# Optimization experiments

Hardware: AMD Instinct MI355X
Metric: run time of the kernel (lower is better)

The kernel has to match this reference:

```python
import jax, jax.numpy as jnp
import numpy as np

N, IN_DIM, HID_DIM, N_CLASSES, MLP_W = 4096, 256, 128, 2, 16


def setup_inputs() -> dict:
    key = jax.random.key(0)
    ks = jax.random.split(key, 8)
    u = jax.random.uniform(ks[0], (N, N), dtype=jnp.float32)
    adj = jnp.where(u < 0.01, 1.0, 0.0).astype(jnp.float32)
    deg_row = adj.sum(axis=1)  # [N]
    deg_col = adj.sum(axis=0)  # [N]
    # per-edge row/col degree features, materialized NxN as in the source
    xdeg = (jnp.broadcast_to(deg_row[:, None], (N, N)) * jnp.ones((1,), jnp.float32)).astype(jnp.float32)
    ydeg = (jnp.broadcast_to(deg_col[None, :], (N, N)) * jnp.ones((1,), jnp.float32)).astype(jnp.float32)
    x = jax.random.normal(ks[1], (N, IN_DIM), dtype=jnp.float32)
    s = 0.1
    We1 = jax.random.normal(ks[2], (3, MLP_W), dtype=jnp.float32) * s
    be1 = jnp.zeros((MLP_W,), jnp.float32)
    We2 = jax.random.normal(ks[3], (MLP_W, 2), dtype=jnp.float32) * s
    be2 = jnp.zeros((2,), jnp.float32)
    W1 = jax.random.normal(ks[4], (IN_DIM, HID_DIM), dtype=jnp.float32) * s
    b1 = jnp.zeros((HID_DIM,), jnp.float32)
    W2 = jax.random.normal(ks[5], (HID_DIM, N_CLASSES), dtype=jnp.float32) * s
    b2 = jnp.zeros((N_CLASSES,), jnp.float32)
    resid_weight = jnp.array(0.5, dtype=jnp.float32)  # learned scalar (init 0.0 in source)
    return {"x": x, "adj": adj, "xdeg": xdeg, "ydeg": ydeg,
            "We1": We1, "be1": be1, "We2": We2, "be2": be2,
            "W1": W1, "b1": b1, "W2": W2, "b2": b2,
            "resid_weight": resid_weight}


def reference(x, adj, xdeg, ydeg, We1, be1, We2, be2, W1, b1, W2, b2, resid_weight):
    n = adj.shape[0]
    # Edge-gating MLP over (adj, xdeg, ydeg). The source gathers nonzero entries,
    # runs the MLP, and scatters back into a zero tensor; computing densely and
    # masking by (adj != 0) is mathematically identical (adj * gate kills zeros).
    feats = jnp.stack([adj, xdeg, ydeg], axis=-1)            # [N, N, 3]
    h = jax.nn.relu(jnp.einsum('nmf,fw->nmw', feats, We1) + be1)  # [N, N, 16]
    gate = jax.nn.softmax(jnp.einsum('nmw,wc->nmc', h, We2) + be2, axis=-1)[..., 1]
    gate = jnp.where(adj != 0.0, gate, 0.0)
    A = adj * gate + jnp.eye(n, dtype=adj.dtype)             # reweighted + self-loops
    # Degree normalization: source does A @ D_col, transpose, @ D_row, transpose,
    # which equals drow[:,None] * A * dcol[None,:]; use broadcasting (no O(N^3) diag mm).
    rs = A.sum(axis=1)
    cs = A.sum(axis=0)
    drow = jnp.where(rs > 0, rs ** -0.5, 0.0)
    dcol = jnp.where(cs > 0, cs ** -0.5, 0.0)
    An = drow[:, None] * A * dcol[None, :]
    # Layer 1: propagate, residual, linear (nn1 = MLP([in, hid]) -> single Linear).
    out = An @ x + resid_weight * x
    hid = out @ W1 + b1
    # dropout is identity in eval mode
    # Layer 2: propagate, residual, classifier.
    out2 = An @ hid + resid_weight * hid
    return out2 @ W2 + b2
```

## Files before the change

kernel.cpp:

```cpp
#include <hip/hip_runtime.h>


typedef unsigned char u8;
typedef unsigned int  u32;

#define N_NODES 4096
#define MAX_DEG 128
#define LUTD    128

__global__ __launch_bounds__(256)
void k_prep(const float* __restrict__ We1, const float* __restrict__ be1,
            const float* __restrict__ We2, const float* __restrict__ be2,
            const float* __restrict__ W1,  const float* __restrict__ b1,
            const float* __restrict__ W2,  const float* __restrict__ b2,
            const float* __restrict__ xdeg, const float* __restrict__ ydeg,
            float* __restrict__ lut, float* __restrict__ M,
            float* __restrict__ cz, float* __restrict__ cfin,
            u8* __restrict__ dc_u8, u8* __restrict__ dr_u8,
            float* __restrict__ cs) {
    int b = blockIdx.x, tid = threadIdx.x;
    if (b < 64) {
        int e = b * 256 + tid;
        float dr = (float)(e >> 7), dc = (float)(e & 127);
        float delta = be2[1] - be2[0];
        #pragma unroll
        for (int w = 0; w < 16; ++w) {
            float hh = fmaf(We1[32 + w], dc,
                       fmaf(We1[16 + w], dr, We1[w] + be1[w]));
            hh = fmaxf(hh, 0.f);
            delta = fmaf(hh, We2[w * 2 + 1] - We2[w * 2], delta);
        }
        lut[e] = 1.f / (1.f + __expf(-delta));
    } else if (b < 66) {
        int e = (b - 64) * 256 + tid;
        int t = e >> 1, d = e & 1;
        float s = 0.f;
        for (int h = 0; h < 128; ++h)
            s = fmaf(W1[t * 128 + h], W2[h * 2 + d], s);
        M[e] = s;
    } else if (b == 66) {
        if (tid < 2) {
            float s = 0.f;
            for (int h = 0; h < 128; ++h)
                s = fmaf(b1[h], W2[h * 2 + tid], s);
            cz[tid]   = s;
            cfin[tid] = b2[tid];
        }
    } else if (b < 83) {
        int j = (b - 67) * 256 + tid;
        int d = (int)ydeg[j];
        dc_u8[j] = (u8)(d > 127 ? 127 : d);
        cs[j] = 0.f;
    } else {
        int i = (b - 83) * 256 + tid;
        int d = (int)xdeg[(size_t)i * N_NODES];
        dr_u8[i] = (u8)(d > 127 ? 127 : d);
    }
}

__global__ __launch_bounds__(256)
void k_gatey(const float* __restrict__ adj, const u8* __restrict__ dr_u8,
             const float* __restrict__ x, const float* __restrict__ lut,
             const u8* __restrict__ dc_u8, const float* __restrict__ M,
             int2* __restrict__ e_g, float* __restrict__ rs,
             float* __restrict__ cs, int* __restrict__ cnt,
             float* __restrict__ y) {
    __shared__ int   s_cnt;
    __shared__ float s_rs[4];
    const int i = blockIdx.x, tid = threadIdx.x;
    const int wv = tid >> 6, lane = tid & 63;
    if (tid == 0) s_cnt = 0;

    const float4* arow4 = (const float4*)(adj + (size_t)i * N_NODES);
    float4 v0 = arow4[tid * 4 + 0];
    float4 v1 = arow4[tid * 4 + 1];
    float4 v2 = arow4[tid * 4 + 2];
    float4 v3 = arow4[tid * 4 + 3];
    uint4  dcw = ((const uint4*)dc_u8)[tid];
    const float* lut_row = lut + (int)dr_u8[i] * LUTD;

    float p0 = 0.f, p1 = 0.f;
    if (wv == 0) {
        float4 xv  = ((const float4*)(x + (size_t)i * 256))[lane];
        float4 m01 = ((const float4*)M)[lane * 2 + 0];
        float4 m23 = ((const float4*)M)[lane * 2 + 1];
        p0 = xv.x * m01.x + xv.y * m01.z + xv.z * m23.x + xv.w * m23.z;
        p1 = xv.x * m01.y + xv.y * m01.w + xv.z * m23.y + xv.w * m23.w;
    }

    float vals[16] = {v0.x, v0.y, v0.z, v0.w, v1.x, v1.y, v1.z, v1.w,
                      v2.x, v2.y, v2.z, v2.w, v3.x, v3.y, v3.z, v3.w};
    u32 mask = 0;
    #pragma unroll
    for (int q = 0; q < 16; ++q)
        mask |= (vals[q] != 0.f) ? (1u << q) : 0u;

    float lrs = 0.f;
    int nloc = __popc(mask);
    if (nloc) {
        int pos = atomicAdd(&s_cnt, nloc);
        int2* er = e_g + (size_t)i * MAX_DEG;
        const u32 w[4] = {dcw.x, dcw.y, dcw.z, dcw.w};
        u32 m = mask;
        while (m) {
            int q = __ffs(m) - 1;
            m &= m - 1;
            int j = tid * 16 + q;
            float gate = lut_row[(w[q >> 2] >> ((q & 3) * 8)) & 255u];
            lrs += gate;
            atomicAdd(cs + j, gate);
            if (pos < MAX_DEG) er[pos] = make_int2(j, __float_as_int(gate));
            ++pos;
        }
    }

    #pragma unroll
    for (int o = 32; o > 0; o >>= 1) {
        lrs += __shfl_down(lrs, o);
        p0  += __shfl_down(p0, o);
        p1  += __shfl_down(p1, o);
    }
    if (lane == 0) s_rs[wv] = lrs;
    if (tid == 0)  ((float2*)y)[i] = make_float2(p0, p1);
    __syncthreads();
    if (tid == 0) {
        rs[i]  = 1.f + s_rs[0] + s_rs[1] + s_rs[2] + s_rs[3];
        cnt[i] = (s_cnt < MAX_DEG) ? s_cnt : MAX_DEG;
    }
}

__global__ __launch_bounds__(256)
void k_spmv(const int2* __restrict__ e_g, const int* __restrict__ cnt,
            const float* __restrict__ rs, const float* __restrict__ cs,
            const float* __restrict__ vin, const float* __restrict__ addv,
            const float* __restrict__ rw, float* __restrict__ vout) {
    int sub = threadIdx.x >> 5, lane32 = threadIdx.x & 31;
    int i = blockIdx.x * 8 + sub;
    int nnz = cnt[i];
    const int2* ep = e_g + (size_t)i * MAX_DEG;
    float a0 = 0.f, a1 = 0.f;
    for (int k = lane32; k < nnz; k += 32) {
        int2 e = ep[k];
        float2 vj = ((const float2*)vin)[e.x];
        float wt = __int_as_float(e.y) * rsqrtf(cs[e.x] + 1.f);
        a0 = fmaf(wt, vj.x, a0);
        a1 = fmaf(wt, vj.y, a1);
    }
    #pragma unroll
    for (int o = 16; o > 0; o >>= 1) {
        a0 += __shfl_down(a0, o, 32);
        a1 += __shfl_down(a1, o, 32);
    }
    if (lane32 == 0) {
        float r  = rw[0];
        float di = rsqrtf(rs[i]), ci = rsqrtf(cs[i] + 1.f);
        float2 yv = ((const float2*)vin)[i];
        float2 o;
        o.x = di * (a0 + ci * yv.x) + r * yv.x + addv[0];
        o.y = di * (a1 + ci * yv.y) + r * yv.y + addv[1];
        ((float2*)vout)[i] = o;
    }
}

extern "C" void kernel_launch(void* const* d_in, const int* in_sizes, int n_in,
                              void* d_out, int out_size, void* d_ws, size_t ws_size,
                              hipStream_t stream) {
    const float* x    = (const float*)d_in[0];
    const float* adj  = (const float*)d_in[1];
    const float* xdeg = (const float*)d_in[2];
    const float* ydeg = (const float*)d_in[3];
    const float* We1  = (const float*)d_in[4];
    const float* be1  = (const float*)d_in[5];
    const float* We2  = (const float*)d_in[6];
    const float* be2  = (const float*)d_in[7];
    const float* W1   = (const float*)d_in[8];
    const float* b1   = (const float*)d_in[9];
    const float* W2   = (const float*)d_in[10];
    const float* b2   = (const float*)d_in[11];
    const float* rw   = (const float*)d_in[12];

    char* ws = (char*)d_ws;
    int2*  e_g  = (int2*) (ws + 0);
    float* lut  = (float*)(ws + 4194304);
    float* rs   = (float*)(ws + 4259840);
    float* cs   = (float*)(ws + 4276224);
    int*   cnt  = (int*)  (ws + 4292608);
    float* y    = (float*)(ws + 4308992);
    float* z    = (float*)(ws + 4341760);
    float* M    = (float*)(ws + 4374528);
    float* cz   = (float*)(ws + 4376576);
    float* cfin = (float*)(ws + 4376584);
    u8*    dcu  = (u8*)   (ws + 4376592);
    u8*    dru  = (u8*)   (ws + 4380688);

    k_prep<<<99, 256, 0, stream>>>(We1, be1, We2, be2, W1, b1, W2, b2, xdeg, ydeg,
                                   lut, M, cz, cfin, dcu, dru, cs);
    k_gatey<<<N_NODES, 256, 0, stream>>>(adj, dru, x, lut, dcu, M,
                                         e_g, rs, cs, cnt, y);
    k_spmv<<<N_NODES / 8, 256, 0, stream>>>(e_g, cnt, rs, cs, y, cz, rw, z);
    k_spmv<<<N_NODES / 8, 256, 0, stream>>>(e_g, cnt, rs, cs, z, cfin, rw, (float*)d_out);
}
```

Baseline: 197.6 us.

## Fuse all stages into one cooperative persistent kernel with grid syncs

Replaces the four launches (prep, gate/edge build, two SpMVs) with one cooperative kernel that runs the same phases separated by grid.sync, using a persistent grid sized from occupancy and capped at 1024 blocks. The gate phase loops over rows, and the SpMV phases give each 64-lane wavefront one row instead of 32-lane subgroups. The aim is to remove launch gaps and tail effects between small kernels. In exchange it adds grid-wide barrier cost and fewer in-flight blocks for streaming the 64MB adjacency matrix, and falls back to the old path if the cooperative launch fails.

```diff
diff --git a/kernel.cpp b/kernel.cpp
--- a/kernel.cpp
+++ b/kernel.cpp
@@ -1,4 +1,7 @@
 #include <hip/hip_runtime.h>
+#include <hip/hip_cooperative_groups.h>
+
+namespace cg = cooperative_groups;
 
 
 typedef unsigned char u8;
@@ -7,6 +10,187 @@
 #define N_NODES 4096
 #define MAX_DEG 128
 #define LUTD    128
+#define NCU     256
+
+
+__device__ __forceinline__ void spmv_phase(
+    const int2* __restrict__ e_g, const int* __restrict__ cnt,
+    const float* __restrict__ rs, const float* __restrict__ cs,
+    const float* __restrict__ vin, float add0, float add1, float rwv,
+    float* __restrict__ vout, int gw, int nwv, int lane)
+{
+    for (int i = gw; i < N_NODES; i += nwv) {
+        int nnz = cnt[i];
+        const int2* ep = e_g + (size_t)i * MAX_DEG;
+        float a0 = 0.f, a1 = 0.f;
+        for (int k = lane; k < nnz; k += 64) {
+            int2 e = ep[k];
+            float2 vj = ((const float2*)vin)[e.x];
+            float wt = __int_as_float(e.y) * rsqrtf(cs[e.x] + 1.f);
+            a0 = fmaf(wt, vj.x, a0);
+            a1 = fmaf(wt, vj.y, a1);
+        }
+        #pragma unroll
+        for (int o = 32; o > 0; o >>= 1) {
+            a0 += __shfl_down(a0, o);
+            a1 += __shfl_down(a1, o);
+        }
+        if (lane == 0) {
+            float di = rsqrtf(rs[i]), ci = rsqrtf(cs[i] + 1.f);
+            float2 yv = ((const float2*)vin)[i];
+            float2 o2;
+            o2.x = di * (a0 + ci * yv.x) + rwv * yv.x + add0;
+            o2.y = di * (a1 + ci * yv.y) + rwv * yv.y + add1;
+            ((float2*)vout)[i] = o2;
+        }
+    }
+}
+
+__global__ __launch_bounds__(256, 4)
+void k_fused(const float* __restrict__ x, const float* __restrict__ adj,
+             const float* __restrict__ xdeg, const float* __restrict__ ydeg,
+             const float* __restrict__ We1, const float* __restrict__ be1,
+             const float* __restrict__ We2, const float* __restrict__ be2,
+             const float* __restrict__ W1,  const float* __restrict__ b1,
+             const float* __restrict__ W2,  const float* __restrict__ b2,
+             const float* __restrict__ rw,  float* __restrict__ outp,
+             char* __restrict__ ws)
+{
+    int2*  e_g  = (int2*) (ws + 0);
+    float* lut  = (float*)(ws + 4194304);
+    float* rs   = (float*)(ws + 4259840);
+    float* cs   = (float*)(ws + 4276224);
+    int*   cnt  = (int*)  (ws + 4292608);
+    float* y    = (float*)(ws + 4308992);
+    float* z    = (float*)(ws + 4341760);
+    float* M    = (float*)(ws + 4374528);
+    float* cz   = (float*)(ws + 4376576);
+    float* cfin = (float*)(ws + 4376584);
+    u8*    dcu  = (u8*)   (ws + 4376592);
+    u8*    dru  = (u8*)   (ws + 4380688);
+
+    cg::grid_group grid = cg::this_grid();
+    const int b = blockIdx.x, tid = threadIdx.x;
+    const int nb = (int)gridDim.x;
+    const int wv = tid >> 6, lane = tid & 63;
+
+    if (b < 64) {
+        int e = b * 256 + tid;
+        float dr = (float)(e >> 7), dc = (float)(e & 127);
+        float delta = be2[1] - be2[0];
+        #pragma unroll
+        for (int w = 0; w < 16; ++w) {
+            float hh = fmaf(We1[32 + w], dc,
+                       fmaf(We1[16 + w], dr, We1[w] + be1[w]));
+            hh = fmaxf(hh, 0.f);
+            delta = fmaf(hh, We2[w * 2 + 1] - We2[w * 2], delta);
+        }
+        lut[e] = 1.f / (1.f + __expf(-delta));
+    } else if (b < 66) {
+        int e = (b - 64) * 256 + tid;
+        int t = e >> 1, d = e & 1;
+        float s = 0.f;
+        for (int h = 0; h < 128; ++h)
+            s = fmaf(W1[t * 128 + h], W2[h * 2 + d], s);
+        M[e] = s;
+    } else if (b == 66) {
+        if (tid < 2) {
+            float s = 0.f;
+            for (int h = 0; h < 128; ++h)
+                s = fmaf(b1[h], W2[h * 2 + tid], s);
+            cz[tid]   = s;
+            cfin[tid] = b2[tid];
+        }
+    } else if (b < 83) {
+        int j = (b - 67) * 256 + tid;
+        int d = (int)ydeg[j];
+        dcu[j] = (u8)(d > 127 ? 127 : d);
+        cs[j] = 0.f;
+    } else if (b < 99) {
+        int i = (b - 83) * 256 + tid;
+        int d = (int)xdeg[(size_t)i * N_NODES];
+        dru[i] = (u8)(d > 127 ? 127 : d);
+    }
+    grid.sync();
+
+    const float rwv = rw[0];
+    const float cz0 = cz[0], cz1 = cz[1];
+    const float cf0 = cfin[0], cf1 = cfin[1];
+    const uint4 dcw = ((const uint4*)dcu)[tid];
+    float4 m01 = {}, m23 = {};
+    if (wv == 0) {
+        m01 = ((const float4*)M)[lane * 2 + 0];
+        m23 = ((const float4*)M)[lane * 2 + 1];
+    }
+
+    __shared__ int   s_cnt;
+    __shared__ float s_rs[4];
+    for (int i = b; i < N_NODES; i += nb) {
+        if (tid == 0) s_cnt = 0;
+        __syncthreads();
+
+        const float4* arow4 = (const float4*)(adj + (size_t)i * N_NODES);
+        float4 v0 = arow4[tid * 4 + 0];
+        float4 v1 = arow4[tid * 4 + 1];
+        float4 v2 = arow4[tid * 4 + 2];
+        float4 v3 = arow4[tid * 4 + 3];
+        const float* lut_row = lut + (int)dru[i] * LUTD;
+
+        float p0 = 0.f, p1 = 0.f;
+        if (wv == 0) {
+            float4 xv = ((const float4*)(x + (size_t)i * 256))[lane];
+            p0 = xv.x * m01.x + xv.y * m01.z + xv.z * m23.x + xv.w * m23.z;
+            p1 = xv.x * m01.y + xv.y * m01.w + xv.z * m23.y + xv.w * m23.w;
+        }
+
+        float vals[16] = {v0.x, v0.y, v0.z, v0.w, v1.x, v1.y, v1.z, v1.w,
+                          v2.x, v2.y, v2.z, v2.w, v3.x, v3.y, v3.z, v3.w};
+        u32 mask = 0;
+        #pragma unroll
+        for (int q = 0; q < 16; ++q)
+            mask |= (vals[q] != 0.f) ? (1u << q) : 0u;
+
+        float lrs = 0.f;
+        int nloc = __popc(mask);
+        if (nloc) {
+            int pos = atomicAdd(&s_cnt, nloc);
+            int2* er = e_g + (size_t)i * MAX_DEG;
+            const u32 w[4] = {dcw.x, dcw.y, dcw.z, dcw.w};
+            u32 m = mask;
+            while (m) {
+                int q = __ffs(m) - 1;
+                m &= m - 1;
+                int j = tid * 16 + q;
+                float gate = lut_row[(w[q >> 2] >> ((q & 3) * 8)) & 255u];
+                lrs += gate;
+                atomicAdd(cs + j, gate);
+                if (pos < MAX_DEG) er[pos] = make_int2(j, __float_as_int(gate));
+                ++pos;
+            }
+        }
+        #pragma unroll
+        for (int o = 32; o > 0; o >>= 1) {
+            lrs += __shfl_down(lrs, o);
+            p0  += __shfl_down(p0, o);
+            p1  += __shfl_down(p1, o);
+        }
+        if (lane == 0) s_rs[wv] = lrs;
+        if (tid == 0)  ((float2*)y)[i] = make_float2(p0, p1);
+        __syncthreads();
+        if (tid == 0) {
+            rs[i]  = 1.f + s_rs[0] + s_rs[1] + s_rs[2] + s_rs[3];
+            cnt[i] = (s_cnt < MAX_DEG) ? s_cnt : MAX_DEG;
+        }
+    }
+    grid.sync();
+
+    const int gw  = b * 4 + wv;
+    const int nwv = nb * 4;
+    spmv_phase(e_g, cnt, rs, cs, y, cz0, cz1, rwv, z, gw, nwv, lane);
+    grid.sync();
+    spmv_phase(e_g, cnt, rs, cs, z, cf0, cf1, rwv, outp, gw, nwv, lane);
+}
+
 
 __global__ __launch_bounds__(256)
 void k_prep(const float* __restrict__ We1, const float* __restrict__ be1,
@@ -178,25 +362,60 @@
     const float* W2   = (const float*)d_in[10];
     const float* b2   = (const float*)d_in[11];
     const float* rw   = (const float*)d_in[12];
-
-    char* ws = (char*)d_ws;
-    int2*  e_g  = (int2*) (ws + 0);
-    float* lut  = (float*)(ws + 4194304);
-    float* rs   = (float*)(ws + 4259840);
-    float* cs   = (float*)(ws + 4276224);
-    int*   cnt  = (int*)  (ws + 4292608);
-    float* y    = (float*)(ws + 4308992);
-    float* z    = (float*)(ws + 4341760);
-    float* M    = (float*)(ws + 4374528);
-    float* cz   = (float*)(ws + 4376576);
-    float* cfin = (float*)(ws + 4376584);
-    u8*    dcu  = (u8*)   (ws + 4376592);
-    u8*    dru  = (u8*)   (ws + 4380688);
-
-    k_prep<<<99, 256, 0, stream>>>(We1, be1, We2, be2, W1, b1, W2, b2, xdeg, ydeg,
-                                   lut, M, cz, cfin, dcu, dru, cs);
-    k_gatey<<<N_NODES, 256, 0, stream>>>(adj, dru, x, lut, dcu, M,
-                                         e_g, rs, cs, cnt, y);
-    k_spmv<<<N_NODES / 8, 256, 0, stream>>>(e_g, cnt, rs, cs, y, cz, rw, z);
-    k_spmv<<<N_NODES / 8, 256, 0, stream>>>(e_g, cnt, rs, cs, z, cfin, rw, (float*)d_out);
-}
+    float* outp = (float*)d_out;
+    char*  ws   = (char*)d_ws;
+
+    static int coop_grid = -2;
+    if (coop_grid == -2) {
+        int nbcu = 0;
+        hipError_t oe = hipOccupancyMaxActiveBlocksPerMultiprocessor(
+            &nbcu, k_fused, 256, 0);
+        if (oe == hipSuccess && nbcu > 0) {
+            int g = nbcu * NCU;
+            if (g > 1024) g = 1024;
+            coop_grid = (g >= 99) ? g : -1;
+        } else {
+            coop_grid = -1;
+            (void)hipGetLastError();
+        }
+    }
+
+    bool done = false;
+    if (coop_grid > 0) {
+        void* kargs[] = {(void*)&x, (void*)&adj, (void*)&xdeg, (void*)&ydeg,
+                         (void*)&We1, (void*)&be1, (void*)&We2, (void*)&be2,
+                         (void*)&W1, (void*)&b1, (void*)&W2, (void*)&b2,
+                         (void*)&rw, (void*)&outp, (void*)&ws};
+        hipError_t e = hipLaunchCooperativeKernel(
+            (const void*)k_fused, dim3(coop_grid), dim3(256), kargs, 0, stream);
+        if (e == hipSuccess) {
+            done = true;
+        } else {
+            coop_grid = -1;
+            (void)hipGetLastError();
+        }
+    }
+
+    if (!done) {
+        int2*  e_g  = (int2*) (ws + 0);
+        float* lut  = (float*)(ws + 4194304);
+        float* rs   = (float*)(ws + 4259840);
+        float* cs   = (float*)(ws + 4276224);
+        int*   cnt  = (int*)  (ws + 4292608);
+        float* y    = (float*)(ws + 4308992);
+        float* z    = (float*)(ws + 4341760);
+        float* M    = (float*)(ws + 4374528);
+        float* cz   = (float*)(ws + 4376576);
+        float* cfin = (float*)(ws + 4376584);
+        u8*    dcu  = (u8*)   (ws + 4376592);
+        u8*    dru  = (u8*)   (ws + 4380688);
+
+        k_prep<<<99, 256, 0, stream>>>(We1, be1, We2, be2, W1, b1, W2, b2,
+                                       xdeg, ydeg, lut, M, cz, cfin, dcu, dru, cs);
+        k_gatey<<<N_NODES, 256, 0, stream>>>(adj, dru, x, lut, dcu, M,
+                                             e_g, rs, cs, cnt, y);
+        k_spmv<<<N_NODES / 8, 256, 0, stream>>>(e_g, cnt, rs, cs, y, cz, rw, z);
+        k_spmv<<<N_NODES / 8, 256, 0, stream>>>(e_g, cnt, rs, cs, z, cfin, rw,
+                                                (float*)d_out);
+    }
+}
```

Measured after the change: 476.6 us. 2.41x slower.
